# Performance work log

Hardware: AMD Instinct MI355X
Metric: run time of the kernel (lower is better)

## Reference

```python
import jax, jax.numpy as jnp
import numpy as np

B, L, H, M, E, NH, R = 4, 512, 1024, 128, 64, 16, 1024   # docs, seq, hidden, mentions, entities, heads, pairs
D, BLK, C = 768, 64, 97                                   # embed_size, block_size, num_class


def setup_inputs() -> dict:
    key = jax.random.key(0)
    ks = jax.random.split(key, 9)
    seq_lhs = jax.random.normal(ks[0], (B, L, H), jnp.float32)
    ent_lhs = jax.random.normal(ks[1], (B, M, H), jnp.float32)
    ent_to_seq_attn = jax.random.uniform(ks[2], (B, NH, M, L), jnp.float32)
    entity_id_labels = jax.random.randint(ks[3], (B, M), 0, E, jnp.int32)
    hts = jax.random.randint(ks[4], (B, R, 2), 0, E, jnp.int32)
    Wh = jax.random.normal(ks[5], (2 * H, D), jnp.float32) * 0.02
    Wt = jax.random.normal(ks[6], (2 * H, D), jnp.float32) * 0.02
    Wb = jax.random.normal(ks[7], (D * BLK, C), jnp.float32) * 0.02
    return dict(seq_lhs=seq_lhs, ent_lhs=ent_lhs, ent_to_seq_attn=ent_to_seq_attn,
                entity_id_labels=entity_id_labels, hts=hts,
                Wh=Wh, bh=jnp.zeros((D,), jnp.float32),
                Wt=Wt, bt=jnp.zeros((D,), jnp.float32),
                Wb=Wb, bb=jnp.zeros((C,), jnp.float32))


def reference(seq_lhs, ent_lhs, ent_to_seq_attn, entity_id_labels, hts, Wh, bh, Wt, bt, Wb, bb):
    # --- hrt_pool: segment logsumexp / mean over mentions per entity ---
    mask = entity_id_labels[:, None, :] == jnp.arange(E, dtype=entity_id_labels.dtype)[None, :, None]  # [B,E,M]
    cnt = mask.sum(-1)  # [B,E]
    neg = jnp.asarray(-1e30, ent_lhs.dtype)
    masked = jnp.where(mask[..., None], ent_lhs[:, None, :, :], neg)          # [B,E,M,H]
    lse = jax.nn.logsumexp(masked, axis=2)                                    # [B,E,H]
    ent_emb = jnp.where((cnt > 0)[..., None], lse, 0.0)
    mf = mask.astype(ent_to_seq_attn.dtype)
    attn_sum = jnp.einsum('bem,bhml->behl', mf, ent_to_seq_attn)              # [B,E,NH,L]
    denom = jnp.maximum(cnt, 1).astype(attn_sum.dtype)[..., None, None]
    ent_attn = jnp.where((cnt > 0)[..., None, None], attn_sum / denom, 0.0)
    # --- gather head/tail entities per pair ---
    h_idx, t_idx = hts[..., 0], hts[..., 1]                                   # [B,R]
    hs = jnp.take_along_axis(ent_emb, h_idx[..., None], axis=1)               # [B,R,H]
    ts = jnp.take_along_axis(ent_emb, t_idx[..., None], axis=1)
    h_attn = jnp.take_along_axis(ent_attn, h_idx[..., None, None], axis=1)    # [B,R,NH,L]
    t_attn = jnp.take_along_axis(ent_attn, t_idx[..., None, None], axis=1)
    ht_attn = (h_attn * t_attn).mean(axis=2)                                  # [B,R,L]
    ht_attn = ht_attn / (ht_attn.sum(-1, keepdims=True) + 1e-5)
    rel = jnp.einsum('brl,bld->brd', ht_attn, seq_lhs)                        # [B,R,H]
    # --- extractors + block bilinear ---
    hcat = jnp.concatenate([hs, rel], -1).reshape(B * R, 2 * H)
    tcat = jnp.concatenate([ts, rel], -1).reshape(B * R, 2 * H)
    hv = jnp.tanh(hcat @ Wh + bh)
    tv = jnp.tanh(tcat @ Wt + bt)
    b1 = hv.reshape(-1, D // BLK, BLK)
    b2 = tv.reshape(-1, D // BLK, BLK)
    bl = (b1[:, :, :, None] * b2[:, :, None, :]).reshape(-1, D * BLK)
    return bl @ Wb + bb                                                       # [B*R, C]
```

## Files before the change

### kernel.cpp

```cpp
#include <hip/hip_runtime.h>
#include <hip/hip_bf16.h>
#include <math.h>

#define B_  4
#define L_  512
#define H_  1024
#define M_  128
#define E_  64
#define NH_ 16
#define R_  1024
#define D_  768
#define BLK_ 64
#define C_  97
#define NROW (B_*R_)
#define KB_  (D_/BLK_)

typedef __attribute__((ext_vector_type(8))) unsigned short ushort8;
typedef __attribute__((ext_vector_type(4))) unsigned short ushort4v;
typedef __attribute__((ext_vector_type(8))) short s8;
typedef __attribute__((ext_vector_type(4))) float f4;

__device__ __forceinline__ unsigned short f2bf(float x) {
    unsigned u = __builtin_bit_cast(unsigned, x);
    unsigned r = (u + 0x7fffu + ((u >> 16) & 1u)) >> 16;
    return (unsigned short)r;
}
__device__ __forceinline__ float bf2f(unsigned short h) {
    unsigned u = ((unsigned)h) << 16;
    return __builtin_bit_cast(float, u);
}
__device__ __forceinline__ float lo16f(unsigned u) { return __builtin_bit_cast(float, u << 16); }
__device__ __forceinline__ float hi16f(unsigned u) { return __builtin_bit_cast(float, u & 0xffff0000u); }

__device__ __forceinline__ void gload_lds16(const unsigned short* g, unsigned short* l)
{
    __builtin_amdgcn_global_load_lds(
        (const __attribute__((address_space(1))) unsigned int*)g,
        (__attribute__((address_space(3))) unsigned int*)l, 16, 0, 0);
}

__global__ __launch_bounds__(256) void pool_lse(
    const float* __restrict__ ent_lhs, const int* __restrict__ labels,
    unsigned short* __restrict__ ent_embB)
{
    int be = blockIdx.x, b = be >> 6, e = be & 63;
    __shared__ int midx[M_];
    __shared__ int scnt;
    if (threadIdx.x == 0) scnt = 0;
    __syncthreads();
    if (threadIdx.x < M_) {
        if (labels[b*M_ + threadIdx.x] == e) {
            int p = atomicAdd(&scnt, 1);
            midx[p] = threadIdx.x;
        }
    }
    __syncthreads();
    int cnt = scnt;
    for (int h = threadIdx.x; h < H_; h += blockDim.x) {
        float r = 0.f;
        if (cnt > 0) {
            const float* base = ent_lhs + (size_t)b*M_*H_ + h;
            float mx = -INFINITY;
            for (int k = 0; k < cnt; ++k) mx = fmaxf(mx, base[(size_t)midx[k]*H_]);
            float s = 0.f;
            for (int k = 0; k < cnt; ++k) s += expf(base[(size_t)midx[k]*H_] - mx);
            r = mx + logf(s);
        }
        ent_embB[(size_t)be*H_ + h] = f2bf(r);
    }
}

__global__ __launch_bounds__(256) void pool_attn(
    const float* __restrict__ attn, const int* __restrict__ labels,
    unsigned short* __restrict__ ent_attnB)
{
    int e  = blockIdx.x;
    int y  = blockIdx.y;
    int b  = y >> 4, nh = y & 15;
    __shared__ int midx[M_];
    __shared__ int scnt;
    if (threadIdx.x == 0) scnt = 0;
    __syncthreads();
    if (threadIdx.x < M_) {
        if (labels[b*M_ + threadIdx.x] == e) {
            int p = atomicAdd(&scnt, 1);
            midx[p] = threadIdx.x;
        }
    }
    __syncthreads();
    int cnt = scnt;
    float inv = (cnt > 0) ? 1.f/(float)cnt : 0.f;
    const float* base = attn + ((size_t)(b*NH_ + nh)*M_)*L_;
    #pragma unroll
    for (int q = 0; q < 2; ++q) {
        int l = threadIdx.x + q*256;
        float s = 0.f;
        for (int k = 0; k < cnt; ++k) s += base[(size_t)midx[k]*L_ + l];
        ent_attnB[((size_t)(b*E_ + e)*NH_ + nh)*L_ + l] = f2bf(s * inv);
    }
}

__global__ __launch_bounds__(256) void pair_attn_kernel(
    const unsigned short* __restrict__ entA, const int* __restrict__ hts,
    unsigned short* __restrict__ htA)
{
    int w  = threadIdx.x >> 6, ln = threadIdx.x & 63;
    int br = blockIdx.x*4 + w, b = br >> 10;
    int hi = hts[br*2 + 0], ti = hts[br*2 + 1];
    const unsigned* ph = (const unsigned*)(entA + ((size_t)(b*E_ + hi)*NH_)*L_);
    const unsigned* pt = (const unsigned*)(entA + ((size_t)(b*E_ + ti)*NH_)*L_);
    float v0[4] = {0.f, 0.f, 0.f, 0.f};
    float v1[4] = {0.f, 0.f, 0.f, 0.f};
    #pragma unroll
    for (int nh = 0; nh < NH_; ++nh) {
        #pragma unroll
        for (int c = 0; c < 4; ++c) {
            int l2 = ln + c*64;
            unsigned a = ph[nh*(L_/2) + l2], d = pt[nh*(L_/2) + l2];
            v0[c] += lo16f(a)*lo16f(d);
            v1[c] += hi16f(a)*hi16f(d);
        }
    }
    float part = 0.f;
    #pragma unroll
    for (int c = 0; c < 4; ++c) part += v0[c] + v1[c];
    #pragma unroll
    for (int off = 32; off > 0; off >>= 1) part += __shfl_xor(part, off, 64);
    float norm = 1.f / (part*(1.f/16.f) + 1e-5f);
    #pragma unroll
    for (int c = 0; c < 4; ++c) {
        unsigned short o0 = f2bf(v0[c]*(1.f/16.f)*norm);
        unsigned short o1 = f2bf(v1[c]*(1.f/16.f)*norm);
        *(unsigned*)(htA + (size_t)br*L_ + (size_t)(ln + c*64)*2) = ((unsigned)o1 << 16) | o0;
    }
}

__global__ __launch_bounds__(256) void transpose_cvt_seq(const float* __restrict__ in,
                                                         unsigned short* __restrict__ outp)
{
    int b = blockIdx.z;
    int h0 = blockIdx.x*32, l0 = blockIdx.y*32;
    __shared__ float tile[32][33];
    int tx = threadIdx.x & 31, ty = threadIdx.x >> 5;
    #pragma unroll
    for (int p = 0; p < 4; ++p)
        tile[ty + p*8][tx] = in[((size_t)b*L_ + l0 + ty + p*8)*H_ + h0 + tx];
    __syncthreads();
    #pragma unroll
    for (int p = 0; p < 4; ++p)
        outp[((size_t)b*H_ + h0 + ty + p*8)*L_ + l0 + tx] = f2bf(tile[tx][ty + p*8]);
}

__global__ __launch_bounds__(256) void transpose_cvt_W(const float* __restrict__ Wh,
                                                       const float* __restrict__ Wt,
                                                       unsigned short* __restrict__ WhT,
                                                       unsigned short* __restrict__ WtT)
{
    const float* in = blockIdx.z ? Wt : Wh;
    unsigned short* outp = blockIdx.z ? WtT : WhT;
    int n0 = blockIdx.x*32, k0 = blockIdx.y*32;
    __shared__ float tile[32][33];
    int tx = threadIdx.x & 31, ty = threadIdx.x >> 5;
    #pragma unroll
    for (int p = 0; p < 4; ++p)
        tile[ty + p*8][tx] = in[((size_t)(k0 + ty + p*8))*D_ + n0 + tx];
    __syncthreads();
    #pragma unroll
    for (int p = 0; p < 4; ++p) {
        int n = n0 + ty + p*8;
        outp[(size_t)n*2048 + k0 + tx] = f2bf(tile[tx][ty + p*8]);
    }
}

__global__ __launch_bounds__(256) void prep_WbT(const float* __restrict__ Wb,
                                                unsigned short* __restrict__ outp)
{
    int blk = blockIdx.x;
    __shared__ float sW[64*97];
    const float* src = Wb + (size_t)blk*64*97;
    for (int e = threadIdx.x; e < 64*97; e += 256) sW[e] = src[e];
    __syncthreads();
    unsigned short* dst = outp + (size_t)blk*128*64;
    for (int e = threadIdx.x; e < 128*64; e += 256) {
        int wcq = e >> 12;
        int ct  = (e >> 10) & 3;
        int j2  = (e >> 9) & 1;
        int qd  = (e >> 7) & 3;
        int lm  = (e >> 3) & 15;
        int t   = e & 7;
        int c   = wcq*64 + ct*16 + lm;
        int j   = j2*32 + qd*8 + t;
        dst[e] = (c < C_) ? f2bf(sW[j*97 + c]) : (unsigned short)0;
    }
}

__device__ __forceinline__ void gemm128_core(const unsigned short* __restrict__ A, int lda,
                                             const unsigned short* __restrict__ Bt, int ldb,
                                             int K, int row0, int col0,
                                             f4 (&acc)[4][4])
{
    __shared__ __attribute__((aligned(16))) unsigned short As[128][32];
    __shared__ __attribute__((aligned(16))) unsigned short Bs[128][32];
    int tid = threadIdx.x;
    int wave = tid >> 6, lane = tid & 63;
    int wr = wave & 1, wc = wave >> 1;
    int lm = lane & 15, quad = lane >> 4;

    for (int k0 = 0; k0 < K; k0 += 32) {
        #pragma unroll
        for (int s = 0; s < 2; ++s) {
            int ch = tid + s*256;
            int row = ch >> 2, part = ch & 3;
            gload_lds16(A  + (size_t)(row0 + row)*lda + k0 + part*8, &As[0][0] + ch*8);
            gload_lds16(Bt + (size_t)(col0 + row)*ldb + k0 + part*8, &Bs[0][0] + ch*8);
        }
        __syncthreads();
        s8 a[4], b[4];
        #pragma unroll
        for (int ti = 0; ti < 4; ++ti) a[ti] = *(const s8*)&As[wr*64 + ti*16 + lm][quad*8];
        #pragma unroll
        for (int tj = 0; tj < 4; ++tj) b[tj] = *(const s8*)&Bs[wc*64 + tj*16 + lm][quad*8];
        #pragma unroll
        for (int ti = 0; ti < 4; ++ti)
            #pragma unroll
            for (int tj = 0; tj < 4; ++tj)
                acc[ti][tj] = __builtin_amdgcn_mfma_f32_16x16x32_bf16(a[ti], b[tj], acc[ti][tj], 0, 0, 0);
        __syncthreads();
    }
}

__global__ __launch_bounds__(256) void gemm_rel_mfma(const unsigned short* __restrict__ htA,
                                                     const unsigned short* __restrict__ seqT,
                                                     unsigned short* __restrict__ relB)
{
    int z = blockIdx.z;
    const unsigned short* A  = htA  + (size_t)z*R_*L_;
    const unsigned short* Bt = seqT + (size_t)z*H_*L_;
    int row0 = blockIdx.y*128, col0 = blockIdx.x*128;
    f4 acc[4][4] = {};
    gemm128_core(A, L_, Bt, L_, L_, row0, col0, acc);
    int lane = threadIdx.x & 63, wave = threadIdx.x >> 6;
    int wr = wave & 1, wc = wave >> 1, lm = lane & 15, quad = lane >> 4;
    #pragma unroll
    for (int ti = 0; ti < 4; ++ti)
        #pragma unroll
        for (int tj = 0; tj < 4; ++tj)
            #pragma unroll
            for (int r = 0; r < 4; ++r) {
                int n   = z*R_ + row0 + wr*64 + ti*16 + quad*4 + r;
                int col = col0 + wc*64 + tj*16 + lm;
                relB[(size_t)n*H_ + col] = f2bf(acc[ti][tj][r]);
            }
}

__global__ __launch_bounds__(256) void gemm_p_mfma(
    const unsigned short* __restrict__ ent_embB,
    const unsigned short* __restrict__ WhT, const unsigned short* __restrict__ WtT,
    float* __restrict__ Ph, float* __restrict__ Pt)
{
    int z = blockIdx.z;
    const unsigned short* Bt = z ? WtT : WhT;
    float* P = z ? Pt : Ph;
    int mt = blockIdx.y & 1, ks = blockIdx.y >> 1;
    int row0 = mt*128, col0 = blockIdx.x*128;
    f4 acc[4][4] = {};
    gemm128_core(ent_embB + ks*256, H_, Bt + ks*256, 2048, 256, row0, col0, acc);
    int lane = threadIdx.x & 63, wave = threadIdx.x >> 6;
    int wr = wave & 1, wc = wave >> 1, lm = lane & 15, quad = lane >> 4;
    #pragma unroll
    for (int ti = 0; ti < 4; ++ti)
        #pragma unroll
        for (int tj = 0; tj < 4; ++tj)
            #pragma unroll
            for (int r = 0; r < 4; ++r) {
                int row = row0 + wr*64 + ti*16 + quad*4 + r;
                int col = col0 + wc*64 + tj*16 + lm;
                atomicAdd(P + (size_t)row*D_ + col, acc[ti][tj][r]);
            }
}

__global__ __launch_bounds__(256) void gemm_ext_mfma(
    const unsigned short* __restrict__ relB,
    const unsigned short* __restrict__ WhT, const unsigned short* __restrict__ WtT,
    const float* __restrict__ Ph, const float* __restrict__ Pt,
    const int* __restrict__ hts,
    float* __restrict__ hv, float* __restrict__ tv)
{
    int z = blockIdx.z;
    const unsigned short* Bt = (z ? WtT : WhT) + 1024;
    const float* P = z ? Pt : Ph;
    float* Cv = z ? tv : hv;
    int row0 = blockIdx.y*128, col0 = blockIdx.x*128;
    f4 acc[4][4] = {};
    gemm128_core(relB, H_, Bt, 2048, H_, row0, col0, acc);
    int lane = threadIdx.x & 63, wave = threadIdx.x >> 6;
    int wr = wave & 1, wc = wave >> 1, lm = lane & 15, quad = lane >> 4;
    #pragma unroll
    for (int ti = 0; ti < 4; ++ti)
        #pragma unroll
        for (int r = 0; r < 4; ++r) {
            int row = row0 + wr*64 + ti*16 + quad*4 + r;
            int b   = row >> 10;
            int idx = hts[row*2 + z];
            const float* prow = P + ((size_t)(b*E_ + idx))*D_;
            #pragma unroll
            for (int tj = 0; tj < 4; ++tj) {
                int col = col0 + wc*64 + tj*16 + lm;
                float x = acc[ti][tj][r] + prow[col];
                float e = __expf(2.f*x);
                Cv[(size_t)row*D_ + col] = 1.f - 2.f/(e + 1.f);
            }
        }
}

__global__ void out_init(const float* __restrict__ bb,
                         const float* __restrict__ bh, const float* __restrict__ bt,
                         float* __restrict__ out,
                         float* __restrict__ Ph, float* __restrict__ Pt)
{
    int i = blockIdx.x*256 + threadIdx.x;
    if (i < NROW*C_) out[i] = bb[i % C_];
    if (i < 256*D_) {
        Ph[i] = bh[i % D_];
        Pt[i] = bt[i % D_];
    }
}

__device__ __forceinline__ void loadB_frag(const unsigned short* __restrict__ bbase,
                                           int i, s8 (&dst)[4][2])
{
    #pragma unroll
    for (int ct = 0; ct < 4; ++ct) {
        dst[ct][0] = *(const s8*)(bbase + (size_t)i*8192 + ct*1024);
        dst[ct][1] = *(const s8*)(bbase + (size_t)i*8192 + ct*1024 + 512);
    }
}

__device__ __forceinline__ void compute_i4(const s8 (&bfr)[4][2],
                                           const float (&sh)[4],
                                           const float (&tvv)[4][2][8],
                                           f4 (&acc)[4][4])
{
    s8 afr[4][2];
    #pragma unroll
    for (int rt = 0; rt < 4; ++rt)
        #pragma unroll
        for (int j2 = 0; j2 < 2; ++j2) {
            union { unsigned u[4]; s8 v; } cv;
            #pragma unroll
            for (int t2 = 0; t2 < 4; ++t2) {
                float pe = sh[rt] * tvv[rt][j2][t2*2];
                float po = sh[rt] * tvv[rt][j2][t2*2 + 1];
                cv.u[t2] = __builtin_amdgcn_perm(__builtin_bit_cast(unsigned, po),
                                                 __builtin_bit_cast(unsigned, pe),
                                                 0x07060302u);
            }
            afr[rt][j2] = cv.v;
        }
    #pragma unroll
    for (int ct = 0; ct < 4; ++ct)
        #pragma unroll
        for (int rt = 0; rt < 4; ++rt) {
            acc[rt][ct] = __builtin_amdgcn_mfma_f32_16x16x32_bf16(afr[rt][0], bfr[ct][0], acc[rt][ct], 0, 0, 0);
            acc[rt][ct] = __builtin_amdgcn_mfma_f32_16x16x32_bf16(afr[rt][1], bfr[ct][1], acc[rt][ct], 0, 0, 0);
        }
}

__global__ __launch_bounds__(256) void final_mfma(
    const float* __restrict__ hv,
    const float* __restrict__ tv,
    const unsigned short* __restrict__ WbT,
    float* __restrict__ out)
{
    int kb   = blockIdx.x;
    int row0 = blockIdx.y * 128;
    __shared__ __attribute__((aligned(16))) unsigned short hS[128][72];
    __shared__ __attribute__((aligned(16))) unsigned short tS[128][72];

    int tid = threadIdx.x;
    for (int e = tid; e < 2048; e += 256) {
        int r = e >> 4, part = e & 15;
        float4 xh = *(const float4*)(hv + (size_t)(row0 + r)*D_ + kb*BLK_ + part*4);
        float4 xt = *(const float4*)(tv + (size_t)(row0 + r)*D_ + kb*BLK_ + part*4);
        ushort4v ph = { f2bf(xh.x), f2bf(xh.y), f2bf(xh.z), f2bf(xh.w) };
        ushort4v pt = { f2bf(xt.x), f2bf(xt.y), f2bf(xt.z), f2bf(xt.w) };
        *(ushort4v*)&hS[r][part*4] = ph;
        *(ushort4v*)&tS[r][part*4] = pt;
    }
    int wave = tid >> 6, lane = tid & 63;
    int wr = wave & 1, wc = wave >> 1;
    int lm = lane & 15, quad = lane >> 4;
    __syncthreads();

    float tvv[4][2][8];
    #pragma unroll
    for (int rt = 0; rt < 4; ++rt)
        #pragma unroll
        for (int j2 = 0; j2 < 2; ++j2) {
            int r = wr*64 + rt*16 + lm;
            ushort8 w = *(const ushort8*)&tS[r][j2*32 + quad*8];
            #pragma unroll
            for (int t = 0; t < 8; ++t) tvv[rt][j2][t] = bf2f(w[t]);
        }

    f4 acc[4][4] = {};
    const unsigned short* bbase = WbT + (size_t)kb*(64*128*64)
                                + (size_t)wc*4096 + ((size_t)quad*16 + lm)*8;

    s8 bufA[4][2], bufB[4][2];
    loadB_frag(bbase, 0, bufA);
    for (int i0 = 0; i0 < 64; i0 += 2) {
        loadB_frag(bbase, i0 + 1, bufB);
        {
            float sh[4];
            #pragma unroll
            for (int rt = 0; rt < 4; ++rt) sh[rt] = bf2f(hS[wr*64 + rt*16 + lm][i0]);
            compute_i4(bufA, sh, tvv, acc);
        }
        if (i0 < 62) loadB_frag(bbase, i0 + 2, bufA);
        {
            float sh[4];
            #pragma unroll
            for (int rt = 0; rt < 4; ++rt) sh[rt] = bf2f(hS[wr*64 + rt*16 + lm][i0 + 1]);
            compute_i4(bufB, sh, tvv, acc);
        }
    }

    #pragma unroll
    for (int rt = 0; rt < 4; ++rt)
        #pragma unroll
        for (int ct = 0; ct < 4; ++ct)
            #pragma unroll
            for (int r = 0; r < 4; ++r) {
                int row = row0 + wr*64 + rt*16 + quad*4 + r;
                int col = wc*64 + ct*16 + lm;
                if (col < C_) atomicAdd(out + (size_t)row*C_ + col, acc[rt][ct][r]);
            }
}

extern "C" void kernel_launch(void* const* d_in, const int* in_sizes, int n_in,
                              void* d_out, int out_size, void* d_ws, size_t ws_size,
                              hipStream_t stream)
{
    const float* seq_lhs = (const float*)d_in[0];
    const float* ent_lhs = (const float*)d_in[1];
    const float* attn    = (const float*)d_in[2];
    const int*   labels  = (const int*)d_in[3];
    const int*   hts     = (const int*)d_in[4];
    const float* Wh      = (const float*)d_in[5];
    const float* bh      = (const float*)d_in[6];
    const float* Wt      = (const float*)d_in[7];
    const float* bt      = (const float*)d_in[8];
    const float* Wb      = (const float*)d_in[9];
    const float* bb      = (const float*)d_in[10];
    float* out = (float*)d_out;

    float* wsf      = (float*)d_ws;
    float* hv       = wsf;
    float* tv       = hv + 3145728;
    float* Ph       = tv + 3145728;
    float* Pt       = Ph + 196608;
    unsigned short* ent_embB  = (unsigned short*)(Pt + 196608);
    unsigned short* ent_attnB = ent_embB  + 262144;
    unsigned short* htA       = ent_attnB + 2097152;
    unsigned short* seqT      = htA       + 2097152;
    unsigned short* WhT       = seqT      + 2097152;
    unsigned short* WtT       = WhT       + 1572864;
    unsigned short* relB      = WtT       + 1572864;
    unsigned short* WbT       = relB      + 4194304;

    transpose_cvt_W<<<dim3(24, 64, 2), 256, 0, stream>>>(Wh, Wt, WhT, WtT);
    prep_WbT<<<KB_*64, 256, 0, stream>>>(Wb, WbT);
    transpose_cvt_seq<<<dim3(32, 16, B_), 256, 0, stream>>>(seq_lhs, seqT);

    pool_lse<<<B_*E_, 256, 0, stream>>>(ent_lhs, labels, ent_embB);
    out_init<<<(NROW*C_ + 255)/256, 256, 0, stream>>>(bb, bh, bt, out, Ph, Pt);
    gemm_p_mfma<<<dim3(6, 8, 2), 256, 0, stream>>>(ent_embB, WhT, WtT, Ph, Pt);
    pool_attn<<<dim3(E_, B_*NH_), 256, 0, stream>>>(attn, labels, ent_attnB);
    pair_attn_kernel<<<B_*R_/4, 256, 0, stream>>>(ent_attnB, hts, htA);
    gemm_rel_mfma<<<dim3(8, 8, B_), 256, 0, stream>>>(htA, seqT, relB);
    gemm_ext_mfma<<<dim3(6, 32, 2), 256, 0, stream>>>(relB, WhT, WtT, Ph, Pt, hts, hv, tv);
    final_mfma<<<dim3(KB_, NROW/128), 256, 0, stream>>>(hv, tv, WbT, out);
}
```

Baseline: 281.8 us.

## Reassociate rel projection: precompute seq·W per doc, then multiply by pair attention

Reorders the matmul chain so seq_lhs is first projected through the rel half of Wh/Wt per document (L×D), and the pair attention matrix then multiplies that product directly. This removes the relB intermediate and the separate rel GEMM, and cuts the FLOPs of the extractor GEMMs (K goes from 1024 to 512). The seq transpose becomes a plain conversion, and hv/tv are stored as bf16 instead of fp32 to shrink the traffic into the final kernel. The price is an extra bf16 rounding of the seq·W product before the attention multiply.

```diff
diff --git a/kernel.cpp b/kernel.cpp
--- a/kernel.cpp
+++ b/kernel.cpp
@@ -135,20 +135,15 @@
     }
 }
 
-__global__ __launch_bounds__(256) void transpose_cvt_seq(const float* __restrict__ in,
-                                                         unsigned short* __restrict__ outp)
-{
-    int b = blockIdx.z;
-    int h0 = blockIdx.x*32, l0 = blockIdx.y*32;
-    __shared__ float tile[32][33];
-    int tx = threadIdx.x & 31, ty = threadIdx.x >> 5;
-    #pragma unroll
-    for (int p = 0; p < 4; ++p)
-        tile[ty + p*8][tx] = in[((size_t)b*L_ + l0 + ty + p*8)*H_ + h0 + tx];
-    __syncthreads();
-    #pragma unroll
-    for (int p = 0; p < 4; ++p)
-        outp[((size_t)b*H_ + h0 + ty + p*8)*L_ + l0 + tx] = f2bf(tile[tx][ty + p*8]);
+__global__ __launch_bounds__(256) void cvt_seq(const float* __restrict__ in,
+                                               unsigned short* __restrict__ outp)
+{
+    size_t i = ((size_t)blockIdx.x*256 + threadIdx.x) * 8;
+    float4 a = *(const float4*)(in + i);
+    float4 b = *(const float4*)(in + i + 4);
+    ushort8 o = { f2bf(a.x), f2bf(a.y), f2bf(a.z), f2bf(a.w),
+                  f2bf(b.x), f2bf(b.y), f2bf(b.z), f2bf(b.w) };
+    *(ushort8*)(outp + i) = o;
 }
 
 __global__ __launch_bounds__(256) void transpose_cvt_W(const float* __restrict__ Wh,
@@ -229,16 +224,18 @@
     }
 }
 
-__global__ __launch_bounds__(256) void gemm_rel_mfma(const unsigned short* __restrict__ htA,
-                                                     const unsigned short* __restrict__ seqT,
-                                                     unsigned short* __restrict__ relB)
-{
-    int z = blockIdx.z;
-    const unsigned short* A  = htA  + (size_t)z*R_*L_;
-    const unsigned short* Bt = seqT + (size_t)z*H_*L_;
+__global__ __launch_bounds__(256) void gemm_swt_mfma(
+    const unsigned short* __restrict__ seqB,
+    const unsigned short* __restrict__ WhT, const unsigned short* __restrict__ WtT,
+    unsigned short* __restrict__ SWT)
+{
+    int bz = blockIdx.z, z = bz >> 2, b = bz & 3;
+    const unsigned short* A  = (z ? WtT : WhT) + 1024;
+    const unsigned short* Bt = seqB + (size_t)b*L_*H_;
     int row0 = blockIdx.y*128, col0 = blockIdx.x*128;
     f4 acc[4][4] = {};
-    gemm128_core(A, L_, Bt, L_, L_, row0, col0, acc);
+    gemm128_core(A, 2048, Bt, H_, H_, row0, col0, acc);
+    unsigned short* Cb = SWT + ((size_t)(z*B_ + b)*D_)*L_;
     int lane = threadIdx.x & 63, wave = threadIdx.x >> 6;
     int wr = wave & 1, wc = wave >> 1, lm = lane & 15, quad = lane >> 4;
     #pragma unroll
@@ -247,9 +244,9 @@
         for (int tj = 0; tj < 4; ++tj)
             #pragma unroll
             for (int r = 0; r < 4; ++r) {
-                int n   = z*R_ + row0 + wr*64 + ti*16 + quad*4 + r;
-                int col = col0 + wc*64 + tj*16 + lm;
-                relB[(size_t)n*H_ + col] = f2bf(acc[ti][tj][r]);
+                int d = row0 + wr*64 + ti*16 + quad*4 + r;
+                int l = col0 + wc*64 + tj*16 + lm;
+                Cb[(size_t)d*L_ + l] = f2bf(acc[ti][tj][r]);
             }
 }
 
@@ -280,19 +277,20 @@
 }
 
 __global__ __launch_bounds__(256) void gemm_ext_mfma(
-    const unsigned short* __restrict__ relB,
-    const unsigned short* __restrict__ WhT, const unsigned short* __restrict__ WtT,
+    const unsigned short* __restrict__ htA,
+    const unsigned short* __restrict__ SWT,
     const float* __restrict__ Ph, const float* __restrict__ Pt,
     const int* __restrict__ hts,
-    float* __restrict__ hv, float* __restrict__ tv)
+    unsigned short* __restrict__ hvB, unsigned short* __restrict__ tvB)
 {
     int z = blockIdx.z;
-    const unsigned short* Bt = (z ? WtT : WhT) + 1024;
     const float* P = z ? Pt : Ph;
-    float* Cv = z ? tv : hv;
+    unsigned short* Cv = z ? tvB : hvB;
     int row0 = blockIdx.y*128, col0 = blockIdx.x*128;
+    int b = row0 >> 10;
+    const unsigned short* Bt = SWT + ((size_t)(z*B_ + b)*D_)*L_;
     f4 acc[4][4] = {};
-    gemm128_core(relB, H_, Bt, 2048, H_, row0, col0, acc);
+    gemm128_core(htA, L_, Bt, L_, L_, row0, col0, acc);
     int lane = threadIdx.x & 63, wave = threadIdx.x >> 6;
     int wr = wave & 1, wc = wave >> 1, lm = lane & 15, quad = lane >> 4;
     #pragma unroll
@@ -300,7 +298,6 @@
         #pragma unroll
         for (int r = 0; r < 4; ++r) {
             int row = row0 + wr*64 + ti*16 + quad*4 + r;
-            int b   = row >> 10;
             int idx = hts[row*2 + z];
             const float* prow = P + ((size_t)(b*E_ + idx))*D_;
             #pragma unroll
@@ -308,7 +305,7 @@
                 int col = col0 + wc*64 + tj*16 + lm;
                 float x = acc[ti][tj][r] + prow[col];
                 float e = __expf(2.f*x);
-                Cv[(size_t)row*D_ + col] = 1.f - 2.f/(e + 1.f);
+                Cv[(size_t)row*D_ + col] = f2bf(1.f - 2.f/(e + 1.f));
             }
         }
 }
@@ -367,8 +364,8 @@
 }
 
 __global__ __launch_bounds__(256) void final_mfma(
-    const float* __restrict__ hv,
-    const float* __restrict__ tv,
+    const unsigned short* __restrict__ hvB,
+    const unsigned short* __restrict__ tvB,
     const unsigned short* __restrict__ WbT,
     float* __restrict__ out)
 {
@@ -378,14 +375,10 @@
     __shared__ __attribute__((aligned(16))) unsigned short tS[128][72];
 
     int tid = threadIdx.x;
-    for (int e = tid; e < 2048; e += 256) {
-        int r = e >> 4, part = e & 15;
-        float4 xh = *(const float4*)(hv + (size_t)(row0 + r)*D_ + kb*BLK_ + part*4);
-        float4 xt = *(const float4*)(tv + (size_t)(row0 + r)*D_ + kb*BLK_ + part*4);
-        ushort4v ph = { f2bf(xh.x), f2bf(xh.y), f2bf(xh.z), f2bf(xh.w) };
-        ushort4v pt = { f2bf(xt.x), f2bf(xt.y), f2bf(xt.z), f2bf(xt.w) };
-        *(ushort4v*)&hS[r][part*4] = ph;
-        *(ushort4v*)&tS[r][part*4] = pt;
+    for (int e = tid; e < 1024; e += 256) {
+        int r = e >> 3, part = e & 7;
+        *(ushort8*)&hS[r][part*8] = *(const ushort8*)(hvB + (size_t)(row0 + r)*D_ + kb*BLK_ + part*8);
+        *(ushort8*)&tS[r][part*8] = *(const ushort8*)(tvB + (size_t)(row0 + r)*D_ + kb*BLK_ + part*8);
     }
     int wave = tid >> 6, lane = tid & 63;
     int wr = wave & 1, wc = wave >> 1;
@@ -456,29 +449,29 @@
     float* out = (float*)d_out;
 
     float* wsf      = (float*)d_ws;
-    float* hv       = wsf;
-    float* tv       = hv + 3145728;
-    float* Ph       = tv + 3145728;
+    float* Ph       = wsf;
     float* Pt       = Ph + 196608;
-    unsigned short* ent_embB  = (unsigned short*)(Pt + 196608);
+    unsigned short* hvB       = (unsigned short*)(Pt + 196608);
+    unsigned short* tvB       = hvB       + 3145728;
+    unsigned short* ent_embB  = tvB       + 3145728;
     unsigned short* ent_attnB = ent_embB  + 262144;
     unsigned short* htA       = ent_attnB + 2097152;
-    unsigned short* seqT      = htA       + 2097152;
-    unsigned short* WhT       = seqT      + 2097152;
+    unsigned short* seqB      = htA       + 2097152;
+    unsigned short* WhT       = seqB      + 2097152;
     unsigned short* WtT       = WhT       + 1572864;
-    unsigned short* relB      = WtT       + 1572864;
-    unsigned short* WbT       = relB      + 4194304;
+    unsigned short* SWT       = WtT       + 1572864;
+    unsigned short* WbT       = SWT       + 3145728;
 
     transpose_cvt_W<<<dim3(24, 64, 2), 256, 0, stream>>>(Wh, Wt, WhT, WtT);
     prep_WbT<<<KB_*64, 256, 0, stream>>>(Wb, WbT);
-    transpose_cvt_seq<<<dim3(32, 16, B_), 256, 0, stream>>>(seq_lhs, seqT);
+    cvt_seq<<<1024, 256, 0, stream>>>(seq_lhs, seqB);
 
     pool_lse<<<B_*E_, 256, 0, stream>>>(ent_lhs, labels, ent_embB);
     out_init<<<(NROW*C_ + 255)/256, 256, 0, stream>>>(bb, bh, bt, out, Ph, Pt);
     gemm_p_mfma<<<dim3(6, 8, 2), 256, 0, stream>>>(ent_embB, WhT, WtT, Ph, Pt);
+    gemm_swt_mfma<<<dim3(4, 6, 8), 256, 0, stream>>>(seqB, WhT, WtT, SWT);
     pool_attn<<<dim3(E_, B_*NH_), 256, 0, stream>>>(attn, labels, ent_attnB);
     pair_attn_kernel<<<B_*R_/4, 256, 0, stream>>>(ent_attnB, hts, htA);
-    gemm_rel_mfma<<<dim3(8, 8, B_), 256, 0, stream>>>(htA, seqT, relB);
-    gemm_ext_mfma<<<dim3(6, 32, 2), 256, 0, stream>>>(relB, WhT, WtT, Ph, Pt, hts, hv, tv);
-    final_mfma<<<dim3(KB_, NROW/128), 256, 0, stream>>>(hv, tv, WbT, out);
-}
+    gemm_ext_mfma<<<dim3(6, 32, 2), 256, 0, stream>>>(htA, SWT, Ph, Pt, hts, hvB, tvB);
+    final_mfma<<<dim3(KB_, NROW/128), 256, 0, stream>>>(hvB, tvB, WbT, out);
+}
```

New measurement: 280.3 us. No clear change (-0.5%).
